# Optimization experiments

Measured on AMD Instinct MI355X. Metric: run time of the kernel, lower is better.

Reference implementation:

```python
import jax, jax.numpy as jnp
import numpy as np


def setup_inputs() -> dict:
    key = jax.random.key(0)
    ks = jax.random.split(key, 5)
    B, C, H, W = 16, 512, 64, 64
    cm = cn = C // 4  # int(C*0.5*0.5)
    # kaiming_normal fan_out for 1x1 conv: std = sqrt(2 / out_channels)
    def kaiming(k, out_c, in_c):
        return jax.random.normal(k, (out_c, in_c), jnp.float32) * np.sqrt(2.0 / out_c)
    return {
        "x": jax.random.normal(ks[0], (B, C, H, W), jnp.float32),
        "WA": kaiming(ks[1], cm, C), "bA": jnp.zeros((cm,), jnp.float32),
        "WB": kaiming(ks[2], cn, C), "bB": jnp.zeros((cn,), jnp.float32),
        "WV": kaiming(ks[3], cn, C), "bV": jnp.zeros((cn,), jnp.float32),
        "WR": kaiming(ks[4], C, cm), "bR": jnp.zeros((C,), jnp.float32),
    }


def reference(x, WA, bA, WB, bB, WV, bV, WR, bR):
    b, c, h, w = x.shape
    n = h * w
    xf = x.reshape(b, c, n)  # [b, c, n] flattened spatial
    # 1x1 convs == per-pixel GEMMs
    A = jnp.einsum('mc,bcn->bmn', WA, xf) + bA[None, :, None]          # [b, cm, n]
    Bm = jax.nn.softmax(jnp.einsum('mc,bcn->bmn', WB, xf) + bB[None, :, None], axis=1)  # softmax over channels
    Vm = jax.nn.softmax(jnp.einsum('mc,bcn->bmn', WV, xf) + bV[None, :, None], axis=1)
    # second-order pooling: global descriptors [b, cm, cn]
    gd = jnp.einsum('bmn,bkn->bmk', A, Bm)
    # distribute: [b, cm, n]
    Z = jnp.einsum('bmk,bkn->bmn', gd, Vm)
    # reconstruct 1x1 conv back to c channels
    out = jnp.einsum('cm,bmn->bcn', WR, Z) + bR[None, :, None]
    return out.reshape(b, c, h, w)
```

## Files before the change

kernel.cpp:

```cpp
#include <hip/hip_runtime.h>
#include <hip/hip_fp16.h>


typedef _Float16 half8 __attribute__((ext_vector_type(8)));
typedef float f32x4 __attribute__((ext_vector_type(4)));

__device__ __forceinline__ unsigned short f2h(float v) {
  return __builtin_bit_cast(unsigned short, (_Float16)v);
}
__device__ __forceinline__ unsigned pk2(float a, float b) {
  return (unsigned)f2h(a) | ((unsigned)f2h(b) << 16);
}
__device__ __forceinline__ f32x4 mfma16(half8 a, half8 b, f32x4 c) {
  return __builtin_amdgcn_mfma_f32_16x16x32_f16(a, b, c, 0, 0, 0);
}
__device__ __forceinline__ int perm32(int v) {
  return (((v & 15) >> 2) << 3) | (((v >> 4) & 1) << 2) | (v & 3);
}
__device__ __forceinline__ void glds16(const unsigned short* g, unsigned short* l) {
  __builtin_amdgcn_global_load_lds(
      (const __attribute__((address_space(1))) unsigned int*)g,
      (__attribute__((address_space(3))) unsigned int*)l, 16, 0, 0);
}
__device__ __forceinline__ half8 ld_frag(const unsigned short* lds, int row) {
  int kg = (threadIdx.x & 63) >> 4;
  uint4 u = *(const uint4*)&lds[(kg * 128 + row) * 8];
  return __builtin_bit_cast(half8, u);
}

__device__ __forceinline__ void stage_glds256(unsigned short* lds,
                                              const unsigned short* g,
                                              int gs, int k0) {
  const int lane = threadIdx.x & 63;
  const int w = threadIdx.x >> 6;
#pragma unroll
  for (int p = 0; p < 2; ++p) {
    int g0 = (w + p * 4) * 64;
    int gi = g0 + lane;
    int row = gi & 127, kg = gi >> 7;
    glds16(g + (size_t)row * gs + k0 + kg * 8, lds + g0 * 8);
  }
}

__global__ __launch_bounds__(256) void k_prep(
    const float* __restrict__ WA, const float* __restrict__ WB,
    const float* __restrict__ WV, const float* __restrict__ WR,
    unsigned short* __restrict__ Wh, unsigned short* __restrict__ WRh) {
  int idx = blockIdx.x * 256 + threadIdx.x;
  if (idx < 196608) {
    int mg = idx >> 16, r = idx & 65535;
    const float* src = (mg == 0) ? WA : ((mg == 1) ? WB : WV);
    Wh[(idx & ~31) | perm32(idx & 31)] = f2h(src[r]);
  } else {
    int r = idx - 196608;
    WRh[(r & ~31) | perm32(r & 31)] = f2h(WR[r]);
  }
}

__global__ __launch_bounds__(384) void k_abv_gd(
    const float* __restrict__ x, const unsigned short* __restrict__ Wh,
    const float* __restrict__ bA, const float* __restrict__ bB,
    const float* __restrict__ bV,
    unsigned short* __restrict__ VmT, float* __restrict__ gdP) {
  const int nt = blockIdx.x, b = blockIdx.y;
  const int tid = threadIdx.x, lane = tid & 63, w = tid >> 6;
  const int kg = lane >> 4, lidx = lane & 15;
  const int mg = w >> 1, wh = w & 1;

  __shared__ unsigned short smem[16384];
  __shared__ float cmaxs[2][2][128], csums[2][2][128];
  __shared__ float sBias[384];

  sBias[tid] = ((mg == 0) ? bA : ((mg == 1) ? bB : bV))[tid & 127];

  const float* xbase = x + (size_t)b * 512 * 4096 + nt * 128;
  const int xn = tid & 127;
  const int xkg = tid >> 7;
  const bool x2 = (tid >= 256);

  float xr[16];

#define XLOAD(K0) do { \
  _Pragma("unroll") for (int j = 0; j < 4; ++j) { \
    xr[j]     = xbase[(size_t)((K0) + 4 * xkg + j) * 4096 + xn]; \
    xr[4 + j] = xbase[(size_t)((K0) + 16 + 4 * xkg + j) * 4096 + xn]; \
  } \
  if (x2) { _Pragma("unroll") for (int j = 0; j < 4; ++j) { \
    xr[8 + j]  = xbase[(size_t)((K0) + 12 + j) * 4096 + xn]; \
    xr[12 + j] = xbase[(size_t)((K0) + 28 + j) * 4096 + xn]; \
  } } } while (0)

#define XWRITE(SX) do { \
  uint4 u_; \
  u_.x = pk2(xr[0], xr[1]); u_.y = pk2(xr[2], xr[3]); \
  u_.z = pk2(xr[4], xr[5]); u_.w = pk2(xr[6], xr[7]); \
  *(uint4*)&(SX)[(xkg * 128 + xn) * 8] = u_; \
  if (x2) { \
    uint4 v_; \
    v_.x = pk2(xr[8], xr[9]);   v_.y = pk2(xr[10], xr[11]); \
    v_.z = pk2(xr[12], xr[13]); v_.w = pk2(xr[14], xr[15]); \
    *(uint4*)&(SX)[(3 * 128 + xn) * 8] = v_; \
  } } while (0)

#define WLOAD(AF, K0) do { \
  _Pragma("unroll") for (int mf_ = 0; mf_ < 4; ++mf_) { \
    const unsigned short* wp_ = Wh + mg * 65536 + \
        (size_t)(wh * 64 + mf_ * 16 + lidx) * 512 + (K0) + kg * 8; \
    (AF)[mf_] = __builtin_bit_cast(half8, *(const uint4*)wp_); \
  } } while (0)

  f32x4 acc[4][8];
#pragma unroll
  for (int mf = 0; mf < 4; ++mf)
#pragma unroll
    for (int nf = 0; nf < 8; ++nf) acc[mf][nf] = (f32x4){0.f, 0.f, 0.f, 0.f};

  half8 afc[4], afn[4];

  XLOAD(0);
  WLOAD(afc, 0);
  XWRITE(smem);

  for (int ks = 0; ks < 16; ++ks) {
    unsigned short* cw = smem + (ks & 1) * 4096;
    unsigned short* nx = smem + ((ks & 1) ^ 1) * 4096;
    __syncthreads();
    if (ks < 15) {
      XLOAD((ks + 1) * 32);
      WLOAD(afn, (ks + 1) * 32);
    }
#pragma unroll
    for (int nf = 0; nf < 8; ++nf) {
      half8 bf = ld_frag(cw, nf * 16 + lidx);
#pragma unroll
      for (int mf = 0; mf < 4; ++mf)
        acc[mf][nf] = mfma16(afc[mf], bf, acc[mf][nf]);
    }
    if (ks < 15) {
      XWRITE(nx);
#pragma unroll
      for (int mf = 0; mf < 4; ++mf) afc[mf] = afn[mf];
    }
  }

#pragma unroll
  for (int mf = 0; mf < 4; ++mf)
#pragma unroll
    for (int i = 0; i < 4; ++i) {
      float bb = sBias[mg * 128 + wh * 64 + mf * 16 + kg * 4 + i];
#pragma unroll
      for (int nf = 0; nf < 8; ++nf) acc[mf][nf][i] += bb;
    }

  float inv_s[8];
  if (mg) {
#pragma unroll
    for (int nf = 0; nf < 8; ++nf) {
      float m = -1e30f;
#pragma unroll
      for (int mf = 0; mf < 4; ++mf)
#pragma unroll
        for (int i = 0; i < 4; ++i) m = fmaxf(m, acc[mf][nf][i]);
      m = fmaxf(m, __shfl_xor(m, 16));
      m = fmaxf(m, __shfl_xor(m, 32));
      if (kg == 0) cmaxs[mg - 1][wh][nf * 16 + lidx] = m;
      inv_s[nf] = m;
    }
  }
  __syncthreads();
  if (mg) {
#pragma unroll
    for (int nf = 0; nf < 8; ++nf) {
      float m = fmaxf(inv_s[nf], cmaxs[mg - 1][wh ^ 1][nf * 16 + lidx]);
      float s = 0.f;
#pragma unroll
      for (int mf = 0; mf < 4; ++mf)
#pragma unroll
        for (int i = 0; i < 4; ++i) {
          float e = __expf(acc[mf][nf][i] - m);
          acc[mf][nf][i] = e;
          s += e;
        }
      s += __shfl_xor(s, 16);
      s += __shfl_xor(s, 32);
      if (kg == 0) csums[mg - 1][wh][nf * 16 + lidx] = s;
      inv_s[nf] = s;
    }
  }
  __syncthreads();
  if (mg) {
#pragma unroll
    for (int nf = 0; nf < 8; ++nf)
      inv_s[nf] = 1.f / (inv_s[nf] + csums[mg - 1][wh ^ 1][nf * 16 + lidx]);
  }

  if (mg == 2) {
    const size_t vofs = ((size_t)b * 4096 + (size_t)nt * 128) * 128;
#pragma unroll
    for (int mf = 0; mf < 4; ++mf) {
      int m0 = wh * 64 + mf * 16 + kg * 4;
      int mp = (m0 & ~31) + perm32(m0 & 31);
#pragma unroll
      for (int nf = 0; nf < 8; ++nf) {
        int n_ = nf * 16 + lidx;
        ushort4 pk;
        pk.x = f2h(acc[mf][nf][0] * inv_s[nf]);
        pk.y = f2h(acc[mf][nf][1] * inv_s[nf]);
        pk.z = f2h(acc[mf][nf][2] * inv_s[nf]);
        pk.w = f2h(acc[mf][nf][3] * inv_s[nf]);
        *(ushort4*)&VmT[vofs + (size_t)n_ * 128 + mp] = pk;
      }
    }
  }

  unsigned short* sA2 = smem;
  unsigned short* sB2 = smem + 8192;
  const int gr = wh, gc = mg;

  f32x4 g2[4][4];
#pragma unroll
  for (int mf = 0; mf < 4; ++mf)
#pragma unroll
    for (int nf = 0; nf < 4; ++nf) g2[mf][nf] = (f32x4){0.f, 0.f, 0.f, 0.f};

#pragma unroll
  for (int r = 0; r < 2; ++r) {
    __syncthreads();
    if (mg != 2) {
      unsigned short* dst = (mg == 0) ? sA2 : sB2;
#pragma unroll
      for (int nfl = 0; nfl < 4; ++nfl) {
        int nf = r * 4 + nfl;
        int base = (nfl >> 1) * 4096 + (lidx >> 2) * 1024 + (nf & 1) * 4 + (lidx & 3);
#pragma unroll
        for (int mf = 0; mf < 4; ++mf)
#pragma unroll
          for (int i = 0; i < 4; ++i) {
            int m_ = wh * 64 + mf * 16 + kg * 4 + i;
            float v = acc[mf][nf][i];
            dst[base + m_ * 8] = f2h(mg ? v * inv_s[nf] : v);
          }
      }
    }
    __syncthreads();
    if (mg != 2) {
#pragma unroll
      for (int ks2 = 0; ks2 < 2; ++ks2) {
        half8 af2[4];
#pragma unroll
        for (int mf = 0; mf < 4; ++mf)
          af2[mf] = ld_frag(sA2 + ks2 * 4096, gr * 64 + mf * 16 + lidx);
#pragma unroll
        for (int nf = 0; nf < 4; ++nf) {
          half8 bf2 = ld_frag(sB2 + ks2 * 4096, gc * 64 + nf * 16 + lidx);
#pragma unroll
          for (int mf = 0; mf < 4; ++mf)
            g2[mf][nf] = mfma16(af2[mf], bf2, g2[mf][nf]);
        }
      }
    }
  }

  if (mg != 2) {
    float* gp = gdP + ((size_t)b * 32 + nt) * 16384;
#pragma unroll
    for (int mf = 0; mf < 4; ++mf)
#pragma unroll
      for (int nf = 0; nf < 4; ++nf) {
        int m0 = gr * 64 + mf * 16 + kg * 4;
        int k2 = gc * 64 + nf * 16 + lidx;
        *(f32x4*)&gp[(size_t)k2 * 128 + m0] = g2[mf][nf];
      }
  }
#undef XLOAD
#undef XWRITE
#undef WLOAD
}

__global__ __launch_bounds__(256) void k_gdred(
    const float* __restrict__ gdP, float* __restrict__ gdT) {
  int gid = blockIdx.x * 256 + threadIdx.x;
  int o = gid * 4;
  int b = o >> 14, rem = o & 16383;
  const float* src = gdP + (size_t)b * 32 * 16384 + rem;
  f32x4 s = (f32x4){0.f, 0.f, 0.f, 0.f};
#pragma unroll 8
  for (int nt = 0; nt < 32; ++nt) s += *(const f32x4*)(src + (size_t)nt * 16384);
  *(f32x4*)(gdT + o) = s;
}

__global__ __launch_bounds__(256) void k_gw(
    const float* __restrict__ gdT, const unsigned short* __restrict__ WRh,
    unsigned short* __restrict__ GWh) {
  const int ct = blockIdx.x, b = blockIdx.y;
  const int tid = threadIdx.x, lane = tid & 63;
  const int w = tid >> 6, wr = w >> 1, wc = w & 1;
  const int kg = lane >> 4, lidx = lane & 15;
  __shared__ unsigned short sG[4096], sWr[4096];
  const float* gb = gdT + (size_t)b * 16384;
  const unsigned short* Wb = WRh + ct * 128 * 128;

  f32x4 acc[4][4];
#pragma unroll
  for (int mf = 0; mf < 4; ++mf)
#pragma unroll
    for (int nf = 0; nf < 4; ++nf) acc[mf][nf] = (f32x4){0.f, 0.f, 0.f, 0.f};

  for (int k0 = 0; k0 < 128; k0 += 32) {
#pragma unroll
    for (int p = 0; p < 2; ++p) {
      int g = tid + p * 256;
      int row = g & 127, kgx = g >> 7;
      const float* s0 = &gb[row * 128 + k0 + 4 * kgx];
      float4 v0 = *(const float4*)s0;
      float4 v1 = *(const float4*)(s0 + 16);
      uint4 u;
      u.x = pk2(v0.x, v0.y); u.y = pk2(v0.z, v0.w);
      u.z = pk2(v1.x, v1.y); u.w = pk2(v1.z, v1.w);
      *(uint4*)&sG[g * 8] = u;
    }
    stage_glds256(sWr, Wb, 128, k0);
    __syncthreads();
    half8 af[4];
#pragma unroll
    for (int mf = 0; mf < 4; ++mf) af[mf] = ld_frag(sG, wr * 64 + mf * 16 + lidx);
#pragma unroll
    for (int nf = 0; nf < 4; ++nf) {
      half8 bf = ld_frag(sWr, wc * 64 + nf * 16 + lidx);
#pragma unroll
      for (int mf = 0; mf < 4; ++mf) acc[mf][nf] = mfma16(af[mf], bf, acc[mf][nf]);
    }
    __syncthreads();
  }
  const size_t gofs = ((size_t)b * 512 + (size_t)ct * 128) * 128;
#pragma unroll
  for (int mf = 0; mf < 4; ++mf) {
    int k0g = wr * 64 + mf * 16 + kg * 4;
    int kp = (k0g & ~31) + perm32(k0g & 31);
#pragma unroll
    for (int nf = 0; nf < 4; ++nf) {
      int c_ = wc * 64 + nf * 16 + lidx;
      ushort4 pk;
      pk.x = f2h(acc[mf][nf][0]); pk.y = f2h(acc[mf][nf][1]);
      pk.z = f2h(acc[mf][nf][2]); pk.w = f2h(acc[mf][nf][3]);
      *(ushort4*)&GWh[gofs + (size_t)c_ * 128 + kp] = pk;
    }
  }
}

__global__ __launch_bounds__(256) void k_out(
    const unsigned short* __restrict__ GWh, const unsigned short* __restrict__ VmT,
    const float* __restrict__ bR, float* __restrict__ out) {
  const int nt = blockIdx.x, ct = blockIdx.y, b = blockIdx.z;
  const int tid = threadIdx.x, lane = tid & 63;
  const int w = tid >> 6, wr = w >> 1, wc = w & 1;
  const int kg = lane >> 4, lidx = lane & 15;
  __shared__ unsigned short sW[4096], sZ[4096];
  __shared__ float sBias[128];
  if (tid < 128) sBias[tid] = bR[ct * 128 + tid];
  const unsigned short* Wb = GWh + ((size_t)b * 512 + (size_t)ct * 128) * 128;
  const unsigned short* Zb = VmT + ((size_t)b * 4096 + (size_t)nt * 128) * 128;

  f32x4 acc[4][4];
#pragma unroll
  for (int mf = 0; mf < 4; ++mf)
#pragma unroll
    for (int nf = 0; nf < 4; ++nf) acc[mf][nf] = (f32x4){0.f, 0.f, 0.f, 0.f};

  for (int k0 = 0; k0 < 128; k0 += 32) {
    stage_glds256(sW, Wb, 128, k0);
    stage_glds256(sZ, Zb, 128, k0);
    __syncthreads();
    half8 af[4];
#pragma unroll
    for (int mf = 0; mf < 4; ++mf) af[mf] = ld_frag(sW, wr * 64 + mf * 16 + lidx);
#pragma unroll
    for (int nf = 0; nf < 4; ++nf) {
      half8 bf = ld_frag(sZ, wc * 64 + nf * 16 + lidx);
#pragma unroll
      for (int mf = 0; mf < 4; ++mf) acc[mf][nf] = mfma16(af[mf], bf, acc[mf][nf]);
    }
    __syncthreads();
  }
#pragma unroll
  for (int mf = 0; mf < 4; ++mf)
#pragma unroll
    for (int nf = 0; nf < 4; ++nf)
#pragma unroll
      for (int i = 0; i < 4; ++i) {
        int cl = wr * 64 + mf * 16 + kg * 4 + i;
        int n_ = nt * 128 + wc * 64 + nf * 16 + lidx;
        out[((size_t)b * 512 + ct * 128 + cl) * 4096 + n_] = acc[mf][nf][i] + sBias[cl];
      }
}

extern "C" void kernel_launch(void* const* d_in, const int* in_sizes, int n_in,
                              void* d_out, int out_size, void* d_ws, size_t ws_size,
                              hipStream_t stream) {
  const float* x  = (const float*)d_in[0];
  const float* WA = (const float*)d_in[1];
  const float* bA = (const float*)d_in[2];
  const float* WB = (const float*)d_in[3];
  const float* bB = (const float*)d_in[4];
  const float* WV = (const float*)d_in[5];
  const float* bV = (const float*)d_in[6];
  const float* WR = (const float*)d_in[7];
  const float* bR = (const float*)d_in[8];
  float* out = (float*)d_out;

  char* ws = (char*)d_ws;
  unsigned short* Wh  = (unsigned short*)(ws);
  unsigned short* WRh = (unsigned short*)(ws + 393216);
  unsigned short* VmT = (unsigned short*)(ws + 524288);
  float*          gdT = (float*)(ws + 17301504);
  unsigned short* GWh = (unsigned short*)(ws + 18350080);
  float*          gdP = (float*)(ws + 20447232);

  k_prep<<<1024, 256, 0, stream>>>(WA, WB, WV, WR, Wh, WRh);
  k_abv_gd<<<dim3(32, 16), 384, 0, stream>>>(x, Wh, bA, bB, bV, VmT, gdP);
  k_gdred<<<256, 256, 0, stream>>>(gdP, gdT);
  k_gw<<<dim3(4, 16), 256, 0, stream>>>(gdT, WRh, GWh);
  k_out<<<dim3(32, 4, 16), 256, 0, stream>>>(GWh, VmT, bR, out);
}
```

Measured before the change: 152.8 us.

## Halve spatial tile in fused ABV/gd kernel to double grid and raise occupancy

```diff
diff --git a/kernel.cpp b/kernel.cpp
--- a/kernel.cpp
+++ b/kernel.cpp
@@ -25,6 +25,11 @@
 __device__ __forceinline__ half8 ld_frag(const unsigned short* lds, int row) {
   int kg = (threadIdx.x & 63) >> 4;
   uint4 u = *(const uint4*)&lds[(kg * 128 + row) * 8];
+  return __builtin_bit_cast(half8, u);
+}
+__device__ __forceinline__ half8 ld_frag64(const unsigned short* lds, int row) {
+  int kg = (threadIdx.x & 63) >> 4;
+  uint4 u = *(const uint4*)&lds[(kg * 64 + row) * 8];
   return __builtin_bit_cast(half8, u);
 }
 
@@ -57,7 +62,7 @@
   }
 }
 
-__global__ __launch_bounds__(384) void k_abv_gd(
+__global__ __launch_bounds__(384, 3) void k_abv_gd(
     const float* __restrict__ x, const unsigned short* __restrict__ Wh,
     const float* __restrict__ bA, const float* __restrict__ bB,
     const float* __restrict__ bV,
@@ -68,38 +73,31 @@
   const int mg = w >> 1, wh = w & 1;
 
   __shared__ unsigned short smem[16384];
-  __shared__ float cmaxs[2][2][128], csums[2][2][128];
+  __shared__ float cmaxs[2][2][64], csums[2][2][64];
   __shared__ float sBias[384];
 
   sBias[tid] = ((mg == 0) ? bA : ((mg == 1) ? bB : bV))[tid & 127];
 
-  const float* xbase = x + (size_t)b * 512 * 4096 + nt * 128;
-  const int xn = tid & 127;
-  const int xkg = tid >> 7;
-  const bool x2 = (tid >= 256);
-
-  float xr[16];
+  const float* xbase = x + (size_t)b * 512 * 4096 + nt * 64;
+  const int xn = tid & 63;
+  const int xkg = (tid >> 6) & 3;
+  const bool xact = (tid < 256);
+
+  float xr[8];
 
 #define XLOAD(K0) do { \
-  _Pragma("unroll") for (int j = 0; j < 4; ++j) { \
-    xr[j]     = xbase[(size_t)((K0) + 4 * xkg + j) * 4096 + xn]; \
-    xr[4 + j] = xbase[(size_t)((K0) + 16 + 4 * xkg + j) * 4096 + xn]; \
-  } \
-  if (x2) { _Pragma("unroll") for (int j = 0; j < 4; ++j) { \
-    xr[8 + j]  = xbase[(size_t)((K0) + 12 + j) * 4096 + xn]; \
-    xr[12 + j] = xbase[(size_t)((K0) + 28 + j) * 4096 + xn]; \
-  } } } while (0)
+  if (xact) { \
+    _Pragma("unroll") for (int j = 0; j < 4; ++j) { \
+      xr[j]     = xbase[(size_t)((K0) + 4 * xkg + j) * 4096 + xn]; \
+      xr[4 + j] = xbase[(size_t)((K0) + 16 + 4 * xkg + j) * 4096 + xn]; \
+    } } } while (0)
 
 #define XWRITE(SX) do { \
-  uint4 u_; \
-  u_.x = pk2(xr[0], xr[1]); u_.y = pk2(xr[2], xr[3]); \
-  u_.z = pk2(xr[4], xr[5]); u_.w = pk2(xr[6], xr[7]); \
-  *(uint4*)&(SX)[(xkg * 128 + xn) * 8] = u_; \
-  if (x2) { \
-    uint4 v_; \
-    v_.x = pk2(xr[8], xr[9]);   v_.y = pk2(xr[10], xr[11]); \
-    v_.z = pk2(xr[12], xr[13]); v_.w = pk2(xr[14], xr[15]); \
-    *(uint4*)&(SX)[(3 * 128 + xn) * 8] = v_; \
+  if (xact) { \
+    uint4 u_; \
+    u_.x = pk2(xr[0], xr[1]); u_.y = pk2(xr[2], xr[3]); \
+    u_.z = pk2(xr[4], xr[5]); u_.w = pk2(xr[6], xr[7]); \
+    *(uint4*)&(SX)[(xkg * 64 + xn) * 8] = u_; \
   } } while (0)
 
 #define WLOAD(AF, K0) do { \
@@ -109,11 +107,11 @@
     (AF)[mf_] = __builtin_bit_cast(half8, *(const uint4*)wp_); \
   } } while (0)
 
-  f32x4 acc[4][8];
+  f32x4 acc[4][4];
 #pragma unroll
   for (int mf = 0; mf < 4; ++mf)
 #pragma unroll
-    for (int nf = 0; nf < 8; ++nf) acc[mf][nf] = (f32x4){0.f, 0.f, 0.f, 0.f};
+    for (int nf = 0; nf < 4; ++nf) acc[mf][nf] = (f32x4){0.f, 0.f, 0.f, 0.f};
 
   half8 afc[4], afn[4];
 
@@ -122,16 +120,16 @@
   XWRITE(smem);
 
   for (int ks = 0; ks < 16; ++ks) {
-    unsigned short* cw = smem + (ks & 1) * 4096;
-    unsigned short* nx = smem + ((ks & 1) ^ 1) * 4096;
+    unsigned short* cw = smem + (ks & 1) * 2048;
+    unsigned short* nx = smem + ((ks & 1) ^ 1) * 2048;
     __syncthreads();
     if (ks < 15) {
       XLOAD((ks + 1) * 32);
       WLOAD(afn, (ks + 1) * 32);
     }
 #pragma unroll
-    for (int nf = 0; nf < 8; ++nf) {
-      half8 bf = ld_frag(cw, nf * 16 + lidx);
+    for (int nf = 0; nf < 4; ++nf) {
+      half8 bf = ld_frag64(cw, nf * 16 + lidx);
 #pragma unroll
       for (int mf = 0; mf < 4; ++mf)
         acc[mf][nf] = mfma16(afc[mf], bf, acc[mf][nf]);
@@ -149,13 +147,13 @@
     for (int i = 0; i < 4; ++i) {
       float bb = sBias[mg * 128 + wh * 64 + mf * 16 + kg * 4 + i];
 #pragma unroll
-      for (int nf = 0; nf < 8; ++nf) acc[mf][nf][i] += bb;
-    }
-
-  float inv_s[8];
+      for (int nf = 0; nf < 4; ++nf) acc[mf][nf][i] += bb;
+    }
+
+  float inv_s[4];
   if (mg) {
 #pragma unroll
-    for (int nf = 0; nf < 8; ++nf) {
+    for (int nf = 0; nf < 4; ++nf) {
       float m = -1e30f;
 #pragma unroll
       for (int mf = 0; mf < 4; ++mf)
@@ -170,7 +168,7 @@
   __syncthreads();
   if (mg) {
 #pragma unroll
-    for (int nf = 0; nf < 8; ++nf) {
+    for (int nf = 0; nf < 4; ++nf) {
       float m = fmaxf(inv_s[nf], cmaxs[mg - 1][wh ^ 1][nf * 16 + lidx]);
       float s = 0.f;
 #pragma unroll
@@ -190,18 +188,36 @@
   __syncthreads();
   if (mg) {
 #pragma unroll
-    for (int nf = 0; nf < 8; ++nf)
+    for (int nf = 0; nf < 4; ++nf)
       inv_s[nf] = 1.f / (inv_s[nf] + csums[mg - 1][wh ^ 1][nf * 16 + lidx]);
   }
 
-  if (mg == 2) {
-    const size_t vofs = ((size_t)b * 4096 + (size_t)nt * 128) * 128;
+  unsigned short* sA2 = smem;
+  unsigned short* sB2 = smem + 8192;
+
+  __syncthreads();
+  if (mg != 2) {
+    unsigned short* dst = (mg == 0) ? sA2 : sB2;
+#pragma unroll
+    for (int nf = 0; nf < 4; ++nf) {
+      int base = (nf >> 1) * 4096 + (lidx >> 2) * 1024 + (nf & 1) * 4 + (lidx & 3);
+#pragma unroll
+      for (int mf = 0; mf < 4; ++mf)
+#pragma unroll
+        for (int i = 0; i < 4; ++i) {
+          int m_ = wh * 64 + mf * 16 + kg * 4 + i;
+          float v = acc[mf][nf][i];
+          dst[base + m_ * 8] = f2h(mg ? v * inv_s[nf] : v);
+        }
+    }
+  } else {
+    const size_t vofs = ((size_t)b * 4096 + (size_t)nt * 64) * 128;
 #pragma unroll
     for (int mf = 0; mf < 4; ++mf) {
       int m0 = wh * 64 + mf * 16 + kg * 4;
       int mp = (m0 & ~31) + perm32(m0 & 31);
 #pragma unroll
-      for (int nf = 0; nf < 8; ++nf) {
+      for (int nf = 0; nf < 4; ++nf) {
         int n_ = nf * 16 + lidx;
         ushort4 pk;
         pk.x = f2h(acc[mf][nf][0] * inv_s[nf]);
@@ -212,57 +228,30 @@
       }
     }
   }
-
-  unsigned short* sA2 = smem;
-  unsigned short* sB2 = smem + 8192;
-  const int gr = wh, gc = mg;
-
-  f32x4 g2[4][4];
-#pragma unroll
-  for (int mf = 0; mf < 4; ++mf)
-#pragma unroll
-    for (int nf = 0; nf < 4; ++nf) g2[mf][nf] = (f32x4){0.f, 0.f, 0.f, 0.f};
-
-#pragma unroll
-  for (int r = 0; r < 2; ++r) {
-    __syncthreads();
-    if (mg != 2) {
-      unsigned short* dst = (mg == 0) ? sA2 : sB2;
-#pragma unroll
-      for (int nfl = 0; nfl < 4; ++nfl) {
-        int nf = r * 4 + nfl;
-        int base = (nfl >> 1) * 4096 + (lidx >> 2) * 1024 + (nf & 1) * 4 + (lidx & 3);
+  __syncthreads();
+
+  if (mg != 2) {
+    const int gr = wh, gc = mg;
+    f32x4 g2[4][4];
+#pragma unroll
+    for (int mf = 0; mf < 4; ++mf)
+#pragma unroll
+      for (int nf = 0; nf < 4; ++nf) g2[mf][nf] = (f32x4){0.f, 0.f, 0.f, 0.f};
+#pragma unroll
+    for (int ks2 = 0; ks2 < 2; ++ks2) {
+      half8 af2[4];
+#pragma unroll
+      for (int mf = 0; mf < 4; ++mf)
+        af2[mf] = ld_frag(sA2 + ks2 * 4096, gr * 64 + mf * 16 + lidx);
+#pragma unroll
+      for (int nf = 0; nf < 4; ++nf) {
+        half8 bf2 = ld_frag(sB2 + ks2 * 4096, gc * 64 + nf * 16 + lidx);
 #pragma unroll
         for (int mf = 0; mf < 4; ++mf)
-#pragma unroll
-          for (int i = 0; i < 4; ++i) {
-            int m_ = wh * 64 + mf * 16 + kg * 4 + i;
-            float v = acc[mf][nf][i];
-            dst[base + m_ * 8] = f2h(mg ? v * inv_s[nf] : v);
-          }
+          g2[mf][nf] = mfma16(af2[mf], bf2, g2[mf][nf]);
       }
     }
-    __syncthreads();
-    if (mg != 2) {
-#pragma unroll
-      for (int ks2 = 0; ks2 < 2; ++ks2) {
-        half8 af2[4];
-#pragma unroll
-        for (int mf = 0; mf < 4; ++mf)
-          af2[mf] = ld_frag(sA2 + ks2 * 4096, gr * 64 + mf * 16 + lidx);
-#pragma unroll
-        for (int nf = 0; nf < 4; ++nf) {
-          half8 bf2 = ld_frag(sB2 + ks2 * 4096, gc * 64 + nf * 16 + lidx);
-#pragma unroll
-          for (int mf = 0; mf < 4; ++mf)
-            g2[mf][nf] = mfma16(af2[mf], bf2, g2[mf][nf]);
-        }
-      }
-    }
-  }
-
-  if (mg != 2) {
-    float* gp = gdP + ((size_t)b * 32 + nt) * 16384;
+    float* gp = gdP + ((size_t)b * 64 + nt) * 16384;
 #pragma unroll
     for (int mf = 0; mf < 4; ++mf)
 #pragma unroll
@@ -282,10 +271,10 @@
   int gid = blockIdx.x * 256 + threadIdx.x;
   int o = gid * 4;
   int b = o >> 14, rem = o & 16383;
-  const float* src = gdP + (size_t)b * 32 * 16384 + rem;
+  const float* src = gdP + (size_t)b * 64 * 16384 + rem;
   f32x4 s = (f32x4){0.f, 0.f, 0.f, 0.f};
 #pragma unroll 8
-  for (int nt = 0; nt < 32; ++nt) s += *(const f32x4*)(src + (size_t)nt * 16384);
+  for (int nt = 0; nt < 64; ++nt) s += *(const f32x4*)(src + (size_t)nt * 16384);
   *(f32x4*)(gdT + o) = s;
 }
 
@@ -417,7 +406,7 @@
   float*          gdP = (float*)(ws + 20447232);
 
   k_prep<<<1024, 256, 0, stream>>>(WA, WB, WV, WR, Wh, WRh);
-  k_abv_gd<<<dim3(32, 16), 384, 0, stream>>>(x, Wh, bA, bB, bV, VmT, gdP);
+  k_abv_gd<<<dim3(64, 16), 384, 0, stream>>>(x, Wh, bA, bB, bV, VmT, gdP);
   k_gdred<<<256, 256, 0, stream>>>(gdP, gdT);
   k_gw<<<dim3(4, 16), 256, 0, stream>>>(gdT, WRh, GWh);
   k_out<<<dim3(32, 4, 16), 256, 0, stream>>>(GWh, VmT, bR, out);
```

Result: slower. 182.9 us (+19.7%).
